# Kernel optimization log

Hardware: AMD Instinct MI355X
Metric: run time of the kernel (lower is better)

## Reference

```python
import jax, jax.numpy as jnp
import numpy as np

N_GRAPHS = 64


def gcn_conv(x, W, b, src, dst, n_nodes):
    """PyG GCNConv: add self-loops, symmetric D^-1/2 (A+I) D^-1/2 normalization,
    linear transform, scatter-add aggregation at target nodes, plus bias."""
    xw = x @ W  # [N, out]  transform before propagate (PyG order)
    loop = jnp.arange(n_nodes, dtype=src.dtype)
    rows = jnp.concatenate([src, loop])  # message sources
    cols = jnp.concatenate([dst, loop])  # message targets
    deg = jax.ops.segment_sum(jnp.ones_like(cols, dtype=xw.dtype), cols,
                              num_segments=n_nodes)
    dinv = jnp.where(deg > 0, jax.lax.rsqrt(deg), 0.0)
    norm = dinv[rows] * dinv[cols]  # [E+N]
    msgs = norm[:, None] * xw[rows]  # gather + scale
    out = jax.ops.segment_sum(msgs, cols, num_segments=n_nodes)  # scatter-add
    return out + b


def global_mean_pool(x, batch, n_graphs):
    sums = jax.ops.segment_sum(x, batch, num_segments=n_graphs)
    cnts = jax.ops.segment_sum(jnp.ones((x.shape[0],), x.dtype), batch,
                               num_segments=n_graphs)
    return sums / jnp.maximum(cnts, 1.0)[:, None]


def setup_inputs() -> dict:
    key = jax.random.key(0)
    k1, k2, k3, k4, k5, k6 = jax.random.split(key, 6)
    N, E = 50000, 800000
    d_in, d_hid, d_out = 128, 128, 64
    x = jax.random.normal(k1, (N, d_in), dtype=jnp.float32)
    edge_index = jax.random.randint(k2, (2, E), 0, N, dtype=jnp.int64)
    batch = jnp.sort(jax.random.randint(k3, (N,), 0, N_GRAPHS, dtype=jnp.int64))
    # Glorot-ish init for GCN weights, zero bias (PyG default)
    W1 = jax.random.normal(k4, (d_in, d_hid), dtype=jnp.float32) / np.sqrt(d_in)
    b1 = jnp.zeros((d_hid,), jnp.float32)
    W2 = jax.random.normal(k5, (d_hid, d_out), dtype=jnp.float32) / np.sqrt(d_hid)
    b2 = jnp.zeros((d_out,), jnp.float32)
    return {"x": x, "edge_index": edge_index, "batch": batch,
            "W1": W1, "b1": b1, "W2": W2, "b2": b2}


def reference(x, edge_index, batch, W1, b1, W2, b2):
    n_nodes = x.shape[0]
    src, dst = edge_index[0], edge_index[1]
    h = jax.nn.relu(gcn_conv(x, W1, b1, src, dst, n_nodes))
    h = gcn_conv(h, W2, b2, src, dst, n_nodes)
    return global_mean_pool(h, batch, N_GRAPHS)
```

## Files before the change

kernel.cpp:

```cpp
#include <hip/hip_runtime.h>

typedef __attribute__((ext_vector_type(8))) short bf16x8;
typedef __attribute__((ext_vector_type(4))) float f32x4;

__device__ __forceinline__ unsigned short f2bf(float f) {
  unsigned u = __float_as_uint(f);
  u += 0x7FFFu + ((u >> 16) & 1u);
  return (unsigned short)(u >> 16);
}
__device__ __forceinline__ float bflo(unsigned u) { return __uint_as_float(u << 16); }
__device__ __forceinline__ float bfhi(unsigned u) { return __uint_as_float(u & 0xFFFF0000u); }

template <int CO, bool AF32, int RT>
__device__ __forceinline__ void gemm_body(const void* __restrict__ Aptr,
                                          const float* __restrict__ W,
                                          unsigned short* __restrict__ Y, int N,
                                          int bid, int tid, unsigned short* Wl) {
  constexpr int K = 128;
  constexpr int SP = K + 8;
  for (int i = tid; i < K * CO; i += 256) {
    int k = i / CO, n = i % CO;
    Wl[n * SP + k] = f2bf(W[i]);
  }
  __syncthreads();

  const int lane = tid & 63;
  const int quad = lane >> 4, l16 = lane & 15;

#pragma unroll
  for (int rt = 0; rt < RT; rt++) {
    const int mbase = bid * (64 * RT) + rt * 64 + (tid >> 6) * 16;
    const int arow = min(mbase + l16, N - 1);

    bf16x8 afrag[4];
    if constexpr (AF32) {
      const float* A = (const float*)Aptr + (size_t)arow * K;
#pragma unroll
      for (int ks = 0; ks < 4; ks++) {
        const float4* p = (const float4*)(A + ks * 32 + quad * 8);
        float4 f0 = p[0], f1 = p[1];
        afrag[ks] = (bf16x8){(short)f2bf(f0.x), (short)f2bf(f0.y), (short)f2bf(f0.z), (short)f2bf(f0.w),
                             (short)f2bf(f1.x), (short)f2bf(f1.y), (short)f2bf(f1.z), (short)f2bf(f1.w)};
      }
    } else {
      const unsigned short* A = (const unsigned short*)Aptr + (size_t)arow * K;
#pragma unroll
      for (int ks = 0; ks < 4; ks++) afrag[ks] = *(const bf16x8*)(A + ks * 32 + quad * 8);
    }

#pragma unroll
    for (int ct = 0; ct < CO / 16; ct++) {
      f32x4 acc = {0.0f, 0.0f, 0.0f, 0.0f};
#pragma unroll
      for (int ks = 0; ks < 4; ks++) {
        bf16x8 b = *(const bf16x8*)(&Wl[(ct * 16 + l16) * SP + ks * 32 + quad * 8]);
        acc = __builtin_amdgcn_mfma_f32_16x16x32_bf16(afrag[ks], b, acc, 0, 0, 0);
      }
#pragma unroll
      for (int reg = 0; reg < 4; reg++) {
        int node = mbase + quad * 4 + reg;
        if (node < N) Y[(size_t)node * CO + ct * 16 + l16] = f2bf(acc[reg]);
      }
    }
  }
}

__global__ __launch_bounds__(256) void k_gemm1(const float* __restrict__ x,
                                               const float* __restrict__ W1,
                                               unsigned short* __restrict__ Y, int N) {
  __shared__ unsigned short Wl[128 * 136];
  gemm_body<128, true, 4>(x, W1, Y, N, blockIdx.x, threadIdx.x, Wl);
}

__global__ __launch_bounds__(256) void k_hist(const int* __restrict__ dst,
                                              int* __restrict__ cnt,
                                              int* __restrict__ rank, int E) {
  const int e0 = (blockIdx.x * 256 + threadIdx.x) * 4;
  if (e0 + 3 < E) {
    int4 d4 = *(const int4*)(dst + e0);
    int4 r;
    r.x = atomicAdd(&cnt[d4.x], 1);
    r.y = atomicAdd(&cnt[d4.y], 1);
    r.z = atomicAdd(&cnt[d4.z], 1);
    r.w = atomicAdd(&cnt[d4.w], 1);
    *(int4*)(rank + e0) = r;
  } else {
    for (int e = e0; e < E; e++) rank[e] = atomicAdd(&cnt[dst[e]], 1);
  }
}

__global__ void k_seg(const int* __restrict__ cnt, int* __restrict__ start,
                      float* __restrict__ dinv, int* __restrict__ counter,
                      const int* __restrict__ batch, int* __restrict__ firstIdx, int N) {
  const int v = blockIdx.x * 256 + threadIdx.x;
  const int lane = threadIdx.x & 63;
  if (v < N) {
    int b = batch[v];
    if (v == 0 || batch[v - 1] != b) firstIdx[b] = v + 1;
  }
  int c = (v < N) ? cnt[v] : 0;
  int incl = c;
#pragma unroll
  for (int d = 1; d < 64; d <<= 1) {
    int t = __shfl_up(incl, d, 64);
    if (lane >= d) incl += t;
  }
  int base = 0;
  if (lane == 63) base = atomicAdd(counter, incl);
  base = __shfl(base, 63, 64);
  if (v < N) {
    start[v] = base + incl - c;
    dinv[v] = rsqrtf((float)(c + 1));
  }
}

__global__ void k_fill(const int* __restrict__ src, const int* __restrict__ dst,
                       const int* __restrict__ rank, const int* __restrict__ start,
                       const float* __restrict__ dinv, int2* __restrict__ colw, int E) {
  int e = blockIdx.x * 256 + threadIdx.x;
  if (e < E) {
    int s = src[e], d = dst[e];
    int p = start[d] + rank[e];
    float w = dinv[s] * dinv[d];
    colw[p] = make_int2(s, __float_as_int(w));
  }
}

__global__ __launch_bounds__(256) void k_agg128(const unsigned short* __restrict__ xwb,
                                                const float* __restrict__ dinv,
                                                const int* __restrict__ start,
                                                const int* __restrict__ cnt,
                                                const int2* __restrict__ colw,
                                                const float* __restrict__ bias,
                                                unsigned short* __restrict__ out, int N) {
  const int tid = threadIdx.x;
  const int lane = tid & 63;
  const int gl = lane & 15;
  const int grp = lane >> 4;
  const int wv = tid >> 6;
  const int v = blockIdx.x * 16 + wv * 4 + grp;
  const int vc = min(v, N - 1);

  const float dv = dinv[vc];
  const int j0 = start[vc];
  const int jc = (v < N) ? cnt[vc] : 0;

  float acc[8];
  {
    const float d2 = dv * dv;
    uint4 s = *(const uint4*)((const char*)xwb + (((size_t)vc << 8) | (gl << 4)));
    acc[0] = d2 * bflo(s.x); acc[1] = d2 * bfhi(s.x);
    acc[2] = d2 * bflo(s.y); acc[3] = d2 * bfhi(s.y);
    acc[4] = d2 * bflo(s.z); acc[5] = d2 * bfhi(s.z);
    acc[6] = d2 * bflo(s.w); acc[7] = d2 * bfhi(s.w);
  }

  const int gbase = grp << 4;
  for (int base = 0; __any(base < jc); base += 16) {
    int2 cw = (base + gl < jc) ? colw[j0 + base + gl] : make_int2(0, 0);
    int mv = jc - base;
    mv = mv < 0 ? 0 : (mv > 16 ? 16 : mv);
    int mm = max(mv, __shfl_xor(mv, 16, 64));
    mm = max(mm, __shfl_xor(mm, 32, 64));
    const int rp = (mm + 3) & ~3;
    for (int t = 0; t < rp; t += 4) {
      uint4 rbuf[4];
      float wbuf[4];
#pragma unroll
      for (int r = 0; r < 4; r++) {
        int sx = __shfl(cw.x, gbase + t + r, 64);
        wbuf[r] = __int_as_float(__shfl(cw.y, gbase + t + r, 64));
        rbuf[r] = *(const uint4*)((const char*)xwb + (((unsigned)sx << 8) | (gl << 4)));
      }
#pragma unroll
      for (int r = 0; r < 4; r++) {
        const float w = wbuf[r];
        const uint4 rr = rbuf[r];
        acc[0] += w * bflo(rr.x); acc[1] += w * bfhi(rr.x);
        acc[2] += w * bflo(rr.y); acc[3] += w * bfhi(rr.y);
        acc[4] += w * bflo(rr.z); acc[5] += w * bfhi(rr.z);
        acc[6] += w * bflo(rr.w); acc[7] += w * bfhi(rr.w);
      }
    }
  }

  if (v < N) {
    float4 b0 = ((const float4*)bias)[gl * 2];
    float4 b1 = ((const float4*)bias)[gl * 2 + 1];
    float a0 = fmaxf(acc[0] + b0.x, 0.f), a1 = fmaxf(acc[1] + b0.y, 0.f);
    float a2 = fmaxf(acc[2] + b0.z, 0.f), a3 = fmaxf(acc[3] + b0.w, 0.f);
    float a4 = fmaxf(acc[4] + b1.x, 0.f), a5 = fmaxf(acc[5] + b1.y, 0.f);
    float a6 = fmaxf(acc[6] + b1.z, 0.f), a7 = fmaxf(acc[7] + b1.w, 0.f);
    uint4 st;
    st.x = (unsigned)f2bf(a0) | ((unsigned)f2bf(a1) << 16);
    st.y = (unsigned)f2bf(a2) | ((unsigned)f2bf(a3) << 16);
    st.z = (unsigned)f2bf(a4) | ((unsigned)f2bf(a5) << 16);
    st.w = (unsigned)f2bf(a6) | ((unsigned)f2bf(a7) << 16);
    *(uint4*)((char*)out + (((size_t)v << 8) | (gl << 4))) = st;
  }
}

__global__ __launch_bounds__(256) void k_gemm2(const unsigned short* __restrict__ A,
                                               const float* __restrict__ W,
                                               unsigned short* __restrict__ Y, int N) {
  __shared__ unsigned short Wl[64 * 136];
  gemm_body<64, false, 4>(A, W, Y, N, blockIdx.x, threadIdx.x, Wl);
}

__global__ __launch_bounds__(256) void k_aggpool(const unsigned short* __restrict__ xwb,
                                                 const float* __restrict__ dinv,
                                                 const int* __restrict__ start,
                                                 const int* __restrict__ cnt,
                                                 const int2* __restrict__ colw,
                                                 const int* __restrict__ batch,
                                                 float* __restrict__ stage, int N) {
  __shared__ float sAcc[4][64];
  const int tid = threadIdx.x;
  const int lane = tid & 63;
  const int gl = lane & 7;
  const int grp = lane >> 3;
  const int wv = tid >> 6;
  const int v = blockIdx.x * 32 + wv * 8 + grp;
  const int vc = min(v, N - 1);

  const float dv = dinv[vc];
  const int j0 = start[vc];
  const int jc = (v < N) ? cnt[vc] : 0;
  const int b = batch[vc];

  float acc[8];
  {
    const float d2 = (v < N) ? dv * dv : 0.0f;
    uint4 s = *(const uint4*)((const char*)xwb + (((size_t)vc << 7) | (gl << 4)));
    acc[0] = d2 * bflo(s.x); acc[1] = d2 * bfhi(s.x);
    acc[2] = d2 * bflo(s.y); acc[3] = d2 * bfhi(s.y);
    acc[4] = d2 * bflo(s.z); acc[5] = d2 * bfhi(s.z);
    acc[6] = d2 * bflo(s.w); acc[7] = d2 * bfhi(s.w);
  }

  const int gbase = grp << 3;
  for (int base = 0; __any(base < jc); base += 8) {
    int2 cw = (base + gl < jc) ? colw[j0 + base + gl] : make_int2(0, 0);
    int mv = jc - base;
    mv = mv < 0 ? 0 : (mv > 8 ? 8 : mv);
    int mm = max(mv, __shfl_xor(mv, 8, 64));
    mm = max(mm, __shfl_xor(mm, 16, 64));
    mm = max(mm, __shfl_xor(mm, 32, 64));
    const int rp = (mm + 3) & ~3;
    for (int t = 0; t < rp; t += 4) {
      uint4 rbuf[4];
      float wbuf[4];
#pragma unroll
      for (int r = 0; r < 4; r++) {
        int sx = __shfl(cw.x, gbase + t + r, 64);
        wbuf[r] = __int_as_float(__shfl(cw.y, gbase + t + r, 64));
        rbuf[r] = *(const uint4*)((const char*)xwb + (((unsigned)sx << 7) | (gl << 4)));
      }
#pragma unroll
      for (int r = 0; r < 4; r++) {
        const float w = wbuf[r];
        const uint4 rr = rbuf[r];
        acc[0] += w * bflo(rr.x); acc[1] += w * bfhi(rr.x);
        acc[2] += w * bflo(rr.y); acc[3] += w * bfhi(rr.y);
        acc[4] += w * bflo(rr.z); acc[5] += w * bfhi(rr.z);
        acc[6] += w * bflo(rr.w); acc[7] += w * bfhi(rr.w);
      }
    }
  }

  const int v0 = blockIdx.x * 32;
  const bool uniform = (v0 + 31 < N) && (batch[v0] == batch[v0 + 31]);
  if (uniform) {
#pragma unroll
    for (int d = 8; d < 64; d <<= 1)
#pragma unroll
      for (int k = 0; k < 8; k++) acc[k] += __shfl_xor(acc[k], d, 64);
    if (grp == 0) {
      *(float4*)&sAcc[wv][gl * 8] = make_float4(acc[0], acc[1], acc[2], acc[3]);
      *(float4*)&sAcc[wv][gl * 8 + 4] = make_float4(acc[4], acc[5], acc[6], acc[7]);
    }
    __syncthreads();
    if (wv == 0) {
      float t = sAcc[0][lane] + sAcc[1][lane] + sAcc[2][lane] + sAcc[3][lane];
      atomicAdd(&stage[batch[v0] * 64 + lane], t);
    }
  } else if (v < N) {
#pragma unroll
    for (int k = 0; k < 8; k++) atomicAdd(&stage[b * 64 + gl * 8 + k], acc[k]);
  }
}

__global__ void k_final(const float* __restrict__ stage, const int* __restrict__ firstIdx,
                        const float* __restrict__ b2, float* __restrict__ out, int N) {
  __shared__ float denom[64];
  const int tid = threadIdx.x;
  if (tid < 64) {
    int raw = firstIdx[tid];
    int fi = (raw > 0) ? raw - 1 : 0x7FFFFFFF;
    int m = fi;
#pragma unroll
    for (int d = 1; d < 64; d <<= 1) {
      int t = __shfl_down(m, d, 64);
      if (tid + d < 64) m = min(m, t);
    }
    int nxtm = __shfl_down(m, 1, 64);
    int nxt = (tid == 63) ? N : min(nxtm, N);
    int c = (fi == 0x7FFFFFFF) ? 0 : (nxt - fi);
    denom[tid] = fmaxf((float)c, 1.0f);
  }
  __syncthreads();
  for (int i = tid; i < 64 * 64; i += 256)
    out[i] = stage[i] / denom[i >> 6] + b2[i & 63];
}


extern "C" void kernel_launch(void* const* d_in, const int* in_sizes, int n_in,
                              void* d_out, int out_size, void* d_ws, size_t ws_size,
                              hipStream_t stream) {
  const float* x     = (const float*)d_in[0];
  const int*   ei    = (const int*)d_in[1];
  const int*   batch = (const int*)d_in[2];
  const float* W1    = (const float*)d_in[3];
  const float* b1    = (const float*)d_in[4];
  const float* W2    = (const float*)d_in[5];
  const float* b2    = (const float*)d_in[6];

  const int N = in_sizes[2];
  const int E = in_sizes[1] / 2;
  const int* src  = ei;
  const int* dstv = ei + E;

  unsigned short* xw1b = (unsigned short*)d_ws;
  unsigned short* h1b  = xw1b + (size_t)N * 128;
  unsigned short* xw2b = xw1b;
  int*   cnt     = (int*)(h1b + (size_t)N * 128);
  int*   counter = cnt + N;
  int*   firstIdx= counter + 1;
  float* stage   = (float*)(firstIdx + 64);
  int*   startv  = (int*)(stage + 4096);
  float* dinv    = (float*)(startv + N);
  int2*  colw    = (int2*)(((uintptr_t)(dinv + N) + 15) & ~(uintptr_t)15);
  int*   rank    = (int*)(colw + E);
  float* outp    = (float*)d_out;

  hipMemsetAsync(cnt, 0, (size_t)(N + 1 + 64 + 4096) * sizeof(int), stream);

  const int gM  = (N + 255) / 256;
  const int gE4 = (E + 1023) / 1024;
  const int gE  = (E + 255) / 256;
  const int gN  = (N + 255) / 256;
  const int gA1 = (N + 15) / 16;
  const int gA2 = (N + 31) / 32;

  k_gemm1<<<gM, 256, 0, stream>>>(x, W1, xw1b, N);
  k_hist<<<gE4, 256, 0, stream>>>(dstv, cnt, rank, E);
  k_seg<<<gN, 256, 0, stream>>>(cnt, startv, dinv, counter, batch, firstIdx, N);
  k_fill<<<gE, 256, 0, stream>>>(src, dstv, rank, startv, dinv, colw, E);

  k_agg128<<<gA1, 256, 0, stream>>>(xw1b, dinv, startv, cnt, colw, b1, h1b, N);

  k_gemm2<<<gM, 256, 0, stream>>>(h1b, W2, xw2b, N);
  k_aggpool<<<gA2, 256, 0, stream>>>(xw2b, dinv, startv, cnt, colw, batch, stage, N);

  k_final<<<1, 256, 0, stream>>>(stage, firstIdx, b2, outp, N);
}
```

Before: 228.4 us.

## Fold symmetric normalization into GEMM outputs and compress CSR to 16-bit indices

Source rows are pre-scaled by dinv inside both GEMM epilogues, and each aggregate is post-scaled by its own dinv. Per-edge weights can therefore be dropped, and the CSR column array becomes 16-bit source indices instead of int2 (index plus weight). This removes per-edge weight stores and loads and the multiplies in the gather loop, and cuts CSR memory traffic. The GEMM now waits for k_seg, so it runs after the degree pass, and a zero padding row at index N serves masked lanes. The 16-bit indices only hold while N stays below 65536.

Measured after the change: 227.2 us. Within noise of the previous version (-0.5%).

```diff
diff --git a/kernel.cpp b/kernel.cpp
--- a/kernel.cpp
+++ b/kernel.cpp
@@ -14,6 +14,7 @@
 template <int CO, bool AF32, int RT>
 __device__ __forceinline__ void gemm_body(const void* __restrict__ Aptr,
                                           const float* __restrict__ W,
+                                          const float* __restrict__ dinv,
                                           unsigned short* __restrict__ Y, int N,
                                           int bid, int tid, unsigned short* Wl) {
   constexpr int K = 128;
@@ -48,6 +49,13 @@
       for (int ks = 0; ks < 4; ks++) afrag[ks] = *(const bf16x8*)(A + ks * 32 + quad * 8);
     }
 
+    float dvr[4];
+#pragma unroll
+    for (int reg = 0; reg < 4; reg++) {
+      int node = mbase + quad * 4 + reg;
+      dvr[reg] = (node < N) ? dinv[node] : 0.0f;
+    }
+
 #pragma unroll
     for (int ct = 0; ct < CO / 16; ct++) {
       f32x4 acc = {0.0f, 0.0f, 0.0f, 0.0f};
@@ -59,17 +67,11 @@
 #pragma unroll
       for (int reg = 0; reg < 4; reg++) {
         int node = mbase + quad * 4 + reg;
-        if (node < N) Y[(size_t)node * CO + ct * 16 + l16] = f2bf(acc[reg]);
-      }
-    }
-  }
-}
-
-__global__ __launch_bounds__(256) void k_gemm1(const float* __restrict__ x,
-                                               const float* __restrict__ W1,
-                                               unsigned short* __restrict__ Y, int N) {
-  __shared__ unsigned short Wl[128 * 136];
-  gemm_body<128, true, 4>(x, W1, Y, N, blockIdx.x, threadIdx.x, Wl);
+        if (node < N) Y[(size_t)node * CO + ct * 16 + l16] = f2bf(acc[reg] * dvr[reg]);
+        else if (node == N) Y[(size_t)node * CO + ct * 16 + l16] = 0;
+      }
+    }
+  }
 }
 
 __global__ __launch_bounds__(256) void k_hist(const int* __restrict__ dst,
@@ -114,15 +116,21 @@
   }
 }
 
+__global__ __launch_bounds__(256) void k_gemm1(const float* __restrict__ x,
+                                               const float* __restrict__ W1,
+                                               const float* __restrict__ dinv,
+                                               unsigned short* __restrict__ Y, int N) {
+  __shared__ unsigned short Wl[128 * 136];
+  gemm_body<128, true, 4>(x, W1, dinv, Y, N, blockIdx.x, threadIdx.x, Wl);
+}
+
 __global__ void k_fill(const int* __restrict__ src, const int* __restrict__ dst,
                        const int* __restrict__ rank, const int* __restrict__ start,
-                       const float* __restrict__ dinv, int2* __restrict__ colw, int E) {
+                       unsigned short* __restrict__ colw16, int E) {
   int e = blockIdx.x * 256 + threadIdx.x;
   if (e < E) {
     int s = src[e], d = dst[e];
-    int p = start[d] + rank[e];
-    float w = dinv[s] * dinv[d];
-    colw[p] = make_int2(s, __float_as_int(w));
+    colw16[start[d] + rank[e]] = (unsigned short)s;
   }
 }
 
@@ -130,7 +138,7 @@
                                                 const float* __restrict__ dinv,
                                                 const int* __restrict__ start,
                                                 const int* __restrict__ cnt,
-                                                const int2* __restrict__ colw,
+                                                const unsigned short* __restrict__ colw16,
                                                 const float* __restrict__ bias,
                                                 unsigned short* __restrict__ out, int N) {
   const int tid = threadIdx.x;
@@ -147,17 +155,16 @@
 
   float acc[8];
   {
-    const float d2 = dv * dv;
     uint4 s = *(const uint4*)((const char*)xwb + (((size_t)vc << 8) | (gl << 4)));
-    acc[0] = d2 * bflo(s.x); acc[1] = d2 * bfhi(s.x);
-    acc[2] = d2 * bflo(s.y); acc[3] = d2 * bfhi(s.y);
-    acc[4] = d2 * bflo(s.z); acc[5] = d2 * bfhi(s.z);
-    acc[6] = d2 * bflo(s.w); acc[7] = d2 * bfhi(s.w);
+    acc[0] = bflo(s.x); acc[1] = bfhi(s.x);
+    acc[2] = bflo(s.y); acc[3] = bfhi(s.y);
+    acc[4] = bflo(s.z); acc[5] = bfhi(s.z);
+    acc[6] = bflo(s.w); acc[7] = bfhi(s.w);
   }
 
   const int gbase = grp << 4;
   for (int base = 0; __any(base < jc); base += 16) {
-    int2 cw = (base + gl < jc) ? colw[j0 + base + gl] : make_int2(0, 0);
+    int cs = (base + gl < jc) ? (int)colw16[j0 + base + gl] : N;
     int mv = jc - base;
     mv = mv < 0 ? 0 : (mv > 16 ? 16 : mv);
     int mm = max(mv, __shfl_xor(mv, 16, 64));
@@ -165,21 +172,18 @@
     const int rp = (mm + 3) & ~3;
     for (int t = 0; t < rp; t += 4) {
       uint4 rbuf[4];
-      float wbuf[4];
 #pragma unroll
       for (int r = 0; r < 4; r++) {
-        int sx = __shfl(cw.x, gbase + t + r, 64);
-        wbuf[r] = __int_as_float(__shfl(cw.y, gbase + t + r, 64));
+        int sx = __shfl(cs, gbase + t + r, 64);
         rbuf[r] = *(const uint4*)((const char*)xwb + (((unsigned)sx << 8) | (gl << 4)));
       }
 #pragma unroll
       for (int r = 0; r < 4; r++) {
-        const float w = wbuf[r];
         const uint4 rr = rbuf[r];
-        acc[0] += w * bflo(rr.x); acc[1] += w * bfhi(rr.x);
-        acc[2] += w * bflo(rr.y); acc[3] += w * bfhi(rr.y);
-        acc[4] += w * bflo(rr.z); acc[5] += w * bfhi(rr.z);
-        acc[6] += w * bflo(rr.w); acc[7] += w * bfhi(rr.w);
+        acc[0] += bflo(rr.x); acc[1] += bfhi(rr.x);
+        acc[2] += bflo(rr.y); acc[3] += bfhi(rr.y);
+        acc[4] += bflo(rr.z); acc[5] += bfhi(rr.z);
+        acc[6] += bflo(rr.w); acc[7] += bfhi(rr.w);
       }
     }
   }
@@ -187,10 +191,10 @@
   if (v < N) {
     float4 b0 = ((const float4*)bias)[gl * 2];
     float4 b1 = ((const float4*)bias)[gl * 2 + 1];
-    float a0 = fmaxf(acc[0] + b0.x, 0.f), a1 = fmaxf(acc[1] + b0.y, 0.f);
-    float a2 = fmaxf(acc[2] + b0.z, 0.f), a3 = fmaxf(acc[3] + b0.w, 0.f);
-    float a4 = fmaxf(acc[4] + b1.x, 0.f), a5 = fmaxf(acc[5] + b1.y, 0.f);
-    float a6 = fmaxf(acc[6] + b1.z, 0.f), a7 = fmaxf(acc[7] + b1.w, 0.f);
+    float a0 = fmaxf(dv * acc[0] + b0.x, 0.f), a1 = fmaxf(dv * acc[1] + b0.y, 0.f);
+    float a2 = fmaxf(dv * acc[2] + b0.z, 0.f), a3 = fmaxf(dv * acc[3] + b0.w, 0.f);
+    float a4 = fmaxf(dv * acc[4] + b1.x, 0.f), a5 = fmaxf(dv * acc[5] + b1.y, 0.f);
+    float a6 = fmaxf(dv * acc[6] + b1.z, 0.f), a7 = fmaxf(dv * acc[7] + b1.w, 0.f);
     uint4 st;
     st.x = (unsigned)f2bf(a0) | ((unsigned)f2bf(a1) << 16);
     st.y = (unsigned)f2bf(a2) | ((unsigned)f2bf(a3) << 16);
@@ -202,16 +206,17 @@
 
 __global__ __launch_bounds__(256) void k_gemm2(const unsigned short* __restrict__ A,
                                                const float* __restrict__ W,
+                                               const float* __restrict__ dinv,
                                                unsigned short* __restrict__ Y, int N) {
   __shared__ unsigned short Wl[64 * 136];
-  gemm_body<64, false, 4>(A, W, Y, N, blockIdx.x, threadIdx.x, Wl);
+  gemm_body<64, false, 4>(A, W, dinv, Y, N, blockIdx.x, threadIdx.x, Wl);
 }
 
 __global__ __launch_bounds__(256) void k_aggpool(const unsigned short* __restrict__ xwb,
                                                  const float* __restrict__ dinv,
                                                  const int* __restrict__ start,
                                                  const int* __restrict__ cnt,
-                                                 const int2* __restrict__ colw,
+                                                 const unsigned short* __restrict__ colw16,
                                                  const int* __restrict__ batch,
                                                  float* __restrict__ stage, int N) {
   __shared__ float sAcc[4][64];
@@ -223,24 +228,23 @@
   const int v = blockIdx.x * 32 + wv * 8 + grp;
   const int vc = min(v, N - 1);
 
-  const float dv = dinv[vc];
+  const float dv = (v < N) ? dinv[vc] : 0.0f;
   const int j0 = start[vc];
   const int jc = (v < N) ? cnt[vc] : 0;
   const int b = batch[vc];
 
   float acc[8];
   {
-    const float d2 = (v < N) ? dv * dv : 0.0f;
     uint4 s = *(const uint4*)((const char*)xwb + (((size_t)vc << 7) | (gl << 4)));
-    acc[0] = d2 * bflo(s.x); acc[1] = d2 * bfhi(s.x);
-    acc[2] = d2 * bflo(s.y); acc[3] = d2 * bfhi(s.y);
-    acc[4] = d2 * bflo(s.z); acc[5] = d2 * bfhi(s.z);
-    acc[6] = d2 * bflo(s.w); acc[7] = d2 * bfhi(s.w);
+    acc[0] = bflo(s.x); acc[1] = bfhi(s.x);
+    acc[2] = bflo(s.y); acc[3] = bfhi(s.y);
+    acc[4] = bflo(s.z); acc[5] = bfhi(s.z);
+    acc[6] = bflo(s.w); acc[7] = bfhi(s.w);
   }
 
   const int gbase = grp << 3;
   for (int base = 0; __any(base < jc); base += 8) {
-    int2 cw = (base + gl < jc) ? colw[j0 + base + gl] : make_int2(0, 0);
+    int cs = (base + gl < jc) ? (int)colw16[j0 + base + gl] : N;
     int mv = jc - base;
     mv = mv < 0 ? 0 : (mv > 8 ? 8 : mv);
     int mm = max(mv, __shfl_xor(mv, 8, 64));
@@ -249,24 +253,24 @@
     const int rp = (mm + 3) & ~3;
     for (int t = 0; t < rp; t += 4) {
       uint4 rbuf[4];
-      float wbuf[4];
 #pragma unroll
       for (int r = 0; r < 4; r++) {
-        int sx = __shfl(cw.x, gbase + t + r, 64);
-        wbuf[r] = __int_as_float(__shfl(cw.y, gbase + t + r, 64));
+        int sx = __shfl(cs, gbase + t + r, 64);
         rbuf[r] = *(const uint4*)((const char*)xwb + (((unsigned)sx << 7) | (gl << 4)));
       }
 #pragma unroll
       for (int r = 0; r < 4; r++) {
-        const float w = wbuf[r];
         const uint4 rr = rbuf[r];
-        acc[0] += w * bflo(rr.x); acc[1] += w * bfhi(rr.x);
-        acc[2] += w * bflo(rr.y); acc[3] += w * bfhi(rr.y);
-        acc[4] += w * bflo(rr.z); acc[5] += w * bfhi(rr.z);
-        acc[6] += w * bflo(rr.w); acc[7] += w * bfhi(rr.w);
-      }
-    }
-  }
+        acc[0] += bflo(rr.x); acc[1] += bfhi(rr.x);
+        acc[2] += bflo(rr.y); acc[3] += bfhi(rr.y);
+        acc[4] += bflo(rr.z); acc[5] += bfhi(rr.z);
+        acc[6] += bflo(rr.w); acc[7] += bfhi(rr.w);
+      }
+    }
+  }
+
+#pragma unroll
+  for (int k = 0; k < 8; k++) acc[k] *= dv;
 
   const int v0 = blockIdx.x * 32;
   const bool uniform = (v0 + 31 < N) && (batch[v0] == batch[v0 + 31]);
@@ -331,7 +335,7 @@
   const int* dstv = ei + E;
 
   unsigned short* xw1b = (unsigned short*)d_ws;
-  unsigned short* h1b  = xw1b + (size_t)N * 128;
+  unsigned short* h1b  = xw1b + (size_t)(N + 1) * 128;
   unsigned short* xw2b = xw1b;
   int*   cnt     = (int*)(h1b + (size_t)N * 128);
   int*   counter = cnt + N;
@@ -339,8 +343,8 @@
   float* stage   = (float*)(firstIdx + 64);
   int*   startv  = (int*)(stage + 4096);
   float* dinv    = (float*)(startv + N);
-  int2*  colw    = (int2*)(((uintptr_t)(dinv + N) + 15) & ~(uintptr_t)15);
-  int*   rank    = (int*)(colw + E);
+  int*   rank    = (int*)(((uintptr_t)(dinv + N) + 15) & ~(uintptr_t)15);
+  unsigned short* colw16 = (unsigned short*)(rank + E);
   float* outp    = (float*)d_out;
 
   hipMemsetAsync(cnt, 0, (size_t)(N + 1 + 64 + 4096) * sizeof(int), stream);
@@ -352,15 +356,15 @@
   const int gA1 = (N + 15) / 16;
   const int gA2 = (N + 31) / 32;
 
-  k_gemm1<<<gM, 256, 0, stream>>>(x, W1, xw1b, N);
   k_hist<<<gE4, 256, 0, stream>>>(dstv, cnt, rank, E);
   k_seg<<<gN, 256, 0, stream>>>(cnt, startv, dinv, counter, batch, firstIdx, N);
-  k_fill<<<gE, 256, 0, stream>>>(src, dstv, rank, startv, dinv, colw, E);
-
-  k_agg128<<<gA1, 256, 0, stream>>>(xw1b, dinv, startv, cnt, colw, b1, h1b, N);
-
-  k_gemm2<<<gM, 256, 0, stream>>>(h1b, W2, xw2b, N);
-  k_aggpool<<<gA2, 256, 0, stream>>>(xw2b, dinv, startv, cnt, colw, batch, stage, N);
+  k_gemm1<<<gM, 256, 0, stream>>>(x, W1, dinv, xw1b, N);
+  k_fill<<<gE, 256, 0, stream>>>(src, dstv, rank, startv, colw16, E);
+
+  k_agg128<<<gA1, 256, 0, stream>>>(xw1b, dinv, startv, cnt, colw16, b1, h1b, N);
+
+  k_gemm2<<<gM, 256, 0, stream>>>(h1b, W2, dinv, xw2b, N);
+  k_aggpool<<<gA2, 256, 0, stream>>>(xw2b, dinv, startv, cnt, colw16, batch, stage, N);
 
   k_final<<<1, 256, 0, stream>>>(stage, firstIdx, b2, outp, N);
 }
```
